# Performance work log

Hardware: AMD Instinct MI355X
Metric: run time of the kernel (lower is better)

## Reference

```python
import jax, jax.numpy as jnp
import numpy as np

DIM, HEADS, DH, M, PINV_ITERS, RES_K = 512, 8, 64, 256, 6, 33

def layernorm(x, w, b, eps=1e-5):
    mu = jnp.mean(x, -1, keepdims=True)
    var = jnp.var(x, -1, keepdims=True)
    return (x - mu) * jax.lax.rsqrt(var + eps) * w + b

def pinv_iter(x, iters=PINV_ITERS):
    # Moore-Penrose iterative pseudo-inverse (lucidrains nystrom-attention)
    ax = jnp.abs(x)
    z = jnp.swapaxes(x, -1, -2) / (jnp.max(ax.sum(-1)) * jnp.max(ax.sum(-2)))
    I = jnp.eye(x.shape[-1], dtype=x.dtype)
    for _ in range(iters):
        xz = x @ z
        z = 0.25 * z @ (13 * I - xz @ (15 * I - xz @ (7 * I - xz)))
    return z

def _core(x, w_qkv):
    b, n, _ = x.shape
    pad = (M - n % M) % M            # Nystrom pads at the FRONT to a multiple of m=256
    xp = jnp.pad(x, ((0, 0), (pad, 0), (0, 0)))
    npad = n + pad
    q, k, v = jnp.split(xp @ w_qkv, 3, axis=-1)
    split_heads = lambda t: t.reshape(b, npad, HEADS, DH).transpose(0, 2, 1, 3)
    q = split_heads(q) * (DH ** -0.5)
    k, v = split_heads(k), split_heads(v)
    l = npad // M                    # tokens per landmark
    q_l = q.reshape(b, HEADS, M, l, DH).mean(3)
    k_l = k.reshape(b, HEADS, M, l, DH).mean(3)
    return q, k, v, q_l, k_l, pad, n

def nystrom_out(x, w_qkv, w_out, b_out, res_kernel):
    q, k, v, q_l, k_l, pad, n = _core(x, w_qkv)
    attn1 = jax.nn.softmax(jnp.einsum('bhid,bhjd->bhij', q, k_l), -1)    # (b,h,N,M)
    attn2 = jax.nn.softmax(jnp.einsum('bhid,bhjd->bhij', q_l, k_l), -1)  # (b,h,M,M)
    attn3 = jax.nn.softmax(jnp.einsum('bhid,bhjd->bhij', q_l, k), -1)    # (b,h,M,N)
    out = (attn1 @ pinv_iter(attn2)) @ (attn3 @ v)
    # depthwise residual conv over sequence dim, per head
    out = out + jax.lax.conv_general_dilated(
        v, res_kernel, (1, 1), [(RES_K // 2, RES_K // 2), (0, 0)],
        dimension_numbers=('NCHW', 'OIHW', 'NCHW'), feature_group_count=HEADS)
    b = out.shape[0]
    out = out.transpose(0, 2, 1, 3).reshape(b, -1, HEADS * DH) @ w_out + b_out
    return out[:, -n:]

def nystrom_cls_row(x, w_qkv):
    # cls-token (query index pad, head 0) row of attn1 @ pinv(attn2) @ attn3;
    # identical math to the full (n x n) matrix row the torch code slices out.
    q, k, v, q_l, k_l, pad, n = _core(x, w_qkv)
    q0, k0, ql0, kl0 = q[:, 0], k[:, 0], q_l[:, 0], k_l[:, 0]
    attn2 = jax.nn.softmax(ql0 @ jnp.swapaxes(kl0, -1, -2), -1)   # (b,M,M)
    attn3 = jax.nn.softmax(ql0 @ jnp.swapaxes(k0, -1, -2), -1)    # (b,M,N)
    row1 = jax.nn.softmax(jnp.einsum('bd,bjd->bj', q0[:, pad], kl0), -1)
    row = jnp.einsum('bj,bjk->bk', row1, pinv_iter(attn2))
    row = jnp.einsum('bk,bkn->bn', row, attn3)                    # (b, N_padded)
    return row, pad

def dwconv(x, k, b, p):
    y = jax.lax.conv_general_dilated(x, k, (1, 1), [(p, p), (p, p)],
        dimension_numbers=('NCHW', 'OIHW', 'NCHW'), feature_group_count=x.shape[1])
    return y + b[None, :, None, None]

def leff(x, k7, b7, k5, b5, k3, b3, Hs, Ws):
    cls_t, feat = x[:, :1], x[:, 1:]
    B, N, C = feat.shape
    img = feat.transpose(0, 2, 1).reshape(B, C, Hs, Ws)
    y = dwconv(img, k7, b7, 3) + img + dwconv(img, k5, b5, 2) + dwconv(img, k3, b3, 1)
    y = y.reshape(B, C, Hs * Ws).transpose(0, 2, 1)
    return jnp.concatenate([cls_t, y], axis=1)

def setup_inputs():
    key = jax.random.key(0)
    ks = iter(jax.random.split(key, 32))
    n, n_classes = 22500, 2
    p = {}
    p['h'] = jax.random.normal(next(ks), (n, 1024), jnp.float32)
    p['fc1_w'] = jax.random.normal(next(ks), (1024, DIM), jnp.float32) * 0.02
    p['fc1_b'] = jnp.zeros((DIM,), jnp.float32)
    p['cls_token'] = jax.random.normal(next(ks), (1, 1, DIM), jnp.float32)
    for pre in ('l1', 'l2'):
        p[pre + '_ln_w'] = jnp.ones((DIM,), jnp.float32)
        p[pre + '_ln_b'] = jnp.zeros((DIM,), jnp.float32)
        p[pre + '_wqkv'] = jax.random.normal(next(ks), (DIM, 3 * HEADS * DH), jnp.float32) * 0.02
        p[pre + '_wout'] = jax.random.normal(next(ks), (HEADS * DH, DIM), jnp.float32) * 0.02
        p[pre + '_bout'] = jnp.zeros((DIM,), jnp.float32)
        p[pre + '_resk'] = jax.random.normal(next(ks), (HEADS, 1, RES_K, 1), jnp.float32) * 0.05
    for kk in (7, 5, 3):
        p['leff_k%d' % kk] = jax.random.normal(next(ks), (DIM, 1, kk, kk), jnp.float32) * 0.05
        p['leff_b%d' % kk] = jnp.zeros((DIM,), jnp.float32)
    p['norm_w'] = jnp.ones((DIM,), jnp.float32)
    p['norm_b'] = jnp.zeros((DIM,), jnp.float32)
    p['fc2_w'] = jax.random.normal(next(ks), (DIM, n_classes), jnp.float32) * 0.02
    p['fc2_b'] = jnp.zeros((n_classes,), jnp.float32)
    return p

def reference(h, fc1_w, fc1_b, cls_token,
              l1_ln_w, l1_ln_b, l1_wqkv, l1_wout, l1_bout, l1_resk,
              leff_k7, leff_b7, leff_k5, leff_b5, leff_k3, leff_b3,
              l2_ln_w, l2_ln_b, l2_wqkv, l2_wout, l2_bout, l2_resk,
              norm_w, norm_b, fc2_w, fc2_b):
    x = h[None]                                   # (1, n, 1024)
    n = x.shape[1]
    x = jax.nn.relu(x @ fc1_w + fc1_b)            # (1, n, 512)
    Hs = int(np.ceil(np.sqrt(n)))                 # 150 for n=22500
    add_len = Hs * Hs - n
    if add_len > 0:
        x = jnp.concatenate([x, x[:, :add_len]], axis=1)
    x = jnp.concatenate([jnp.broadcast_to(cls_token, (1, 1, DIM)), x], axis=1)
    # TransLayer 1
    x = x + nystrom_out(layernorm(x, l1_ln_w, l1_ln_b), l1_wqkv, l1_wout, l1_bout, l1_resk)
    # LeFF positional layer
    x = leff(x, leff_k7, leff_b7, leff_k5, leff_b5, leff_k3, leff_b3, Hs, Hs)
    # TransLayer 2 (first call in TransMIL.forward)
    h2 = x + nystrom_out(layernorm(x, l2_ln_w, l2_ln_b), l2_wqkv, l2_wout, l2_bout, l2_resk)
    # TransLayer 2 second call: residual update then attention matrix of updated state
    h3 = h2 + nystrom_out(layernorm(h2, l2_ln_w, l2_ln_b), l2_wqkv, l2_wout, l2_bout, l2_resk)
    row, pad = nystrom_cls_row(layernorm(h3, l2_ln_w, l2_ln_b), l2_wqkv)
    A = row[0, pad + 1: pad + 1 + n][:, None]     # (n, 1) cls->instance attention
    hf = layernorm(h2, norm_w, norm_b)[:, 0]      # (1, 512)
    logits = hf @ fc2_w + fc2_b                   # (1, n_classes)
    Y_prob = jax.nn.softmax(logits, -1)
    return logits, Y_prob, A
```

## Files before the change

### kernel.cpp

```cpp
#include <hip/hip_runtime.h>

#define NTOK 22500
#define N1   22501
#define NPAD 22528
#define PADR 27
#define DIM  512
#define NH   8
#define DHD  64
#define MM   256
#define LLM  88
#define HSZ  150
#define CSZ  256
#define NCH  88

typedef short bf16x8 __attribute__((ext_vector_type(8)));
typedef float f32x4  __attribute__((ext_vector_type(4)));
typedef unsigned short us;

union U8 { bf16x8 v; unsigned short u[8]; };

__device__ __forceinline__ unsigned short f2b(float f){
  unsigned int u = __float_as_uint(f);
  unsigned int r = u + 0x7fffu + ((u>>16)&1u);
  return (unsigned short)(r>>16);
}
__device__ __forceinline__ float bf2f(unsigned short u){
  return __uint_as_float(((unsigned int)u)<<16);
}
__device__ __forceinline__ bf16x8 cvt8(float4 a, float4 b){
  U8 u;
  u.u[0]=f2b(a.x); u.u[1]=f2b(a.y); u.u[2]=f2b(a.z); u.u[3]=f2b(a.w);
  u.u[4]=f2b(b.x); u.u[5]=f2b(b.y); u.u[6]=f2b(b.z); u.u[7]=f2b(b.w);
  return u.v;
}
__device__ __forceinline__ void gld16(const void* g, void* l){
  __builtin_amdgcn_global_load_lds(
      (const __attribute__((address_space(1))) void*)g,
      (__attribute__((address_space(3))) void*)l, 16, 0, 0);
}

__device__ __forceinline__ float waveSum(float v){
#pragma unroll
  for (int o=32;o>0;o>>=1) v += __shfl_down(v,o);
  return v;
}
__device__ __forceinline__ float waveMax(float v){
#pragma unroll
  for (int o=32;o>0;o>>=1) v = fmaxf(v,__shfl_down(v,o));
  return v;
}
__device__ __forceinline__ float blockSum256(float v, float* sb){
  v = waveSum(v);
  __syncthreads();
  if ((threadIdx.x&63)==0) sb[threadIdx.x>>6]=v;
  __syncthreads();
  return sb[0]+sb[1]+sb[2]+sb[3];
}
__device__ __forceinline__ float blockMax256(float v, float* sb){
  v = waveMax(v);
  __syncthreads();
  if ((threadIdx.x&63)==0) sb[threadIdx.x>>6]=v;
  __syncthreads();
  return fmaxf(fmaxf(sb[0],sb[1]),fmaxf(sb[2],sb[3]));
}

__global__ void k_wT(const float* __restrict__ W, us* __restrict__ Bt, int K, int N)
{
  __shared__ float tile[32][33];
  int tx = threadIdx.x&31, ty = threadIdx.x>>5;
  int k0 = blockIdx.x*32, n0 = blockIdx.y*32;
#pragma unroll
  for (int i=0;i<4;++i){
    int k = k0+ty+i*8;
    if (k<K && n0+tx<N) tile[ty+i*8][tx] = W[(size_t)k*N + n0+tx];
  }
  __syncthreads();
#pragma unroll
  for (int i=0;i<4;++i){
    int n = n0+ty+i*8, k = k0+tx;
    if (n<N && k<K) Bt[(size_t)n*K + k] = f2b(tile[tx][ty+i*8]);
  }
}

__global__ void k_vT(const us* __restrict__ V, us* __restrict__ Vt)
{
  __shared__ us tile[32][33];
  int tx = threadIdx.x&31, ty = threadIdx.x>>5;
  int p0 = blockIdx.x*32;
  int h = blockIdx.y>>1, d0 = (blockIdx.y&1)*32;
#pragma unroll
  for (int i=0;i<4;++i){
    int p = p0+ty+i*8;
    tile[ty+i*8][tx] = V[((size_t)h*NPAD+p)*DHD + d0+tx];
  }
  __syncthreads();
#pragma unroll
  for (int i=0;i<4;++i){
    int d = d0+ty+i*8;
    Vt[((size_t)h*DHD+d)*NPAD + p0+tx] = tile[tx][ty+i*8];
  }
}

template<int MODE>
__global__ __launch_bounds__(256) void k_gemm(const float* __restrict__ Af,
    const us* __restrict__ Ab, const us* __restrict__ Bt, const float* __restrict__ bias,
    us* __restrict__ Xb, float* __restrict__ Cf, float* __restrict__ C2,
    us* __restrict__ Q_, us* __restrict__ K_, us* __restrict__ V_,
    const us* __restrict__ zpg, int Kd)
{
  __shared__ us SM[16384];
  us* As = SM;
  us* Bs = SM + 8192;
  const int tid = threadIdx.x;
  const int m0 = blockIdx.x*128, n0 = blockIdx.y*128;
  const int lane = tid & 63;
  const int wid = tid >> 6;
  const int wm = (wid>>1)*64, wn = (wid&1)*64;
  f32x4 acc[4][4] = {};
  for (int k0=0; k0<Kd; k0+=64){
    __syncthreads();
    if (MODE==0){
#pragma unroll
      for (int i=0;i<8;++i){
        int g = i*256 + tid;
        int row = g>>4, k4 = (g&15)*4;
        int gm = m0 + row;
        ushort4 h4 = make_ushort4(0,0,0,0);
        if (gm < NTOK){
          float4 v = *(const float4*)(Af + (size_t)gm*Kd + k0 + k4);
          h4.x=f2b(v.x); h4.y=f2b(v.y); h4.z=f2b(v.z); h4.w=f2b(v.w);
        }
        *(ushort4*)(&As[row*64 + (k4 ^ ((row&7)<<3))]) = h4;
      }
    } else {
#pragma unroll
      for (int i=0;i<4;++i){
        int c = wid*4+i;
        int row = c*8 + (lane>>3);
        int scol8 = ((lane&7) ^ (row&7))*8;
        int gm = m0+row;
        const us* ga;
        if (MODE==2) ga = Ab + ((size_t)((gm<N1?gm:0)+PADR))*Kd + k0 + scol8;
        else ga = (gm>=PADR) ? Ab + (size_t)(gm-PADR)*Kd + k0 + scol8 : zpg + scol8;
        gld16(ga, &As[c*512]);
      }
    }
#pragma unroll
    for (int i=0;i<4;++i){
      int c = wid*4+i;
      int row = c*8 + (lane>>3);
      int scol8 = ((lane&7) ^ (row&7))*8;
      int vn = n0+row;
      if (MODE==3) vn = (vn<64)? vn : vn+448;
      gld16(Bt + (size_t)vn*Kd + k0 + scol8, &Bs[c*512]);
    }
    __syncthreads();
#pragma unroll
    for (int ks=0; ks<2; ++ks){
      const int kk = ks*32 + (lane>>4)*8;
      bf16x8 af[4], bfm[4];
#pragma unroll
      for (int t=0;t<4;++t){
        int r = wm + t*16 + (lane&15);
        af[t] = *(bf16x8*)(&As[r*64 + (kk ^ ((r&7)<<3))]);
        int c = wn + t*16 + (lane&15);
        bfm[t] = *(bf16x8*)(&Bs[c*64 + (kk ^ ((c&7)<<3))]);
      }
#pragma unroll
      for (int mt=0;mt<4;++mt)
#pragma unroll
        for (int nt=0;nt<4;++nt)
          acc[mt][nt] = __builtin_amdgcn_mfma_f32_16x16x32_bf16(af[mt], bfm[nt], acc[mt][nt], 0,0,0);
    }
  }
  const int rbase = (lane>>4)*4;
  const int cl = lane&15;
  if (MODE==3){
#pragma unroll
    for (int mt=0;mt<4;++mt)
#pragma unroll
      for (int r=0;r<4;++r){
        int gm = m0 + wm + mt*16 + rbase + r;
#pragma unroll
        for (int nt=0;nt<4;++nt){
          int gn = n0 + wn + nt*16 + cl;
          float v = acc[mt][nt][r];
          if (gn < 64) Cf[(size_t)gm*DHD + gn] = v*0.125f;
          else         C2[(size_t)gm*DHD + (gn-64)] = v;
        }
      }
    return;
  }
  const float sc1 = (MODE==1 && (blockIdx.y>>2)==0) ? 0.125f : 1.f;
  __syncthreads();
#pragma unroll
  for (int mt=0;mt<4;++mt)
#pragma unroll
    for (int r=0;r<4;++r){
      int row = wm + mt*16 + rbase + r;
#pragma unroll
      for (int nt=0;nt<4;++nt){
        int col = wn + nt*16 + cl;
        float v = acc[mt][nt][r];
        if (MODE==0){ v += bias[n0+col]; v = v>0.f?v:0.f; }
        else if (MODE==2){ v += bias[n0+col]; }
        else v *= sc1;
        SM[row*128 + col] = f2b(v);
      }
    }
  __syncthreads();
  if (MODE==1){
    const int sec = blockIdx.y>>2;
    us* dst = sec==0 ? Q_ : (sec==1 ? K_ : V_);
#pragma unroll
    for (int i=0;i<8;++i){
      int v8 = i*256 + tid;
      int row = v8>>4, c8 = (v8&15)*8;
      int gm = m0 + row, gn = n0 + c8;
      int hh = (gn>>6)&7, d = gn&63;
      *(bf16x8*)(dst + ((size_t)hh*NPAD+gm)*DHD + d) = *(bf16x8*)(&SM[row*128 + c8]);
    }
  } else if (MODE==0){
#pragma unroll
    for (int i=0;i<8;++i){
      int v8 = i*256 + tid;
      int row = v8>>4, c8 = (v8&15)*8;
      int gm = m0 + row;
      if (gm < NTOK)
        *(bf16x8*)(Xb + (size_t)(1+gm)*DIM + n0 + c8) = *(bf16x8*)(&SM[row*128 + c8]);
    }
  } else {
#pragma unroll
    for (int i=0;i<8;++i){
      int v8 = i*256 + tid;
      int row = v8>>4, c8 = (v8&15)*8;
      int gm = m0 + row;
      if (gm < N1){
        us* p = Xb + (size_t)gm*DIM + n0 + c8;
        U8 xo, ad, o;
        xo.v = *(bf16x8*)p;
        ad.v = *(bf16x8*)(&SM[row*128 + c8]);
#pragma unroll
        for (int j=0;j<8;++j) o.u[j] = f2b(bf2f(xo.u[j]) + bf2f(ad.u[j]));
        *(bf16x8*)p = o.v;
      }
    }
  }
}

__global__ void k_setcls(us* __restrict__ X, const float* __restrict__ cls){
  int i = blockIdx.x*256 + threadIdx.x;
  if (i < DIM) X[i] = f2b(cls[i]);
}
__global__ void k_copyu(us* __restrict__ d, const us* __restrict__ s, size_t n){
  size_t i = (size_t)blockIdx.x*256 + threadIdx.x;
  if (i<n) d[i]=s[i];
}

__global__ void k_ln(const us* __restrict__ X, us* __restrict__ Y,
                     const float* __restrict__ w, const float* __restrict__ b)
{
  __shared__ float sb[4];
  const us* x = X + (size_t)blockIdx.x*DIM;
  us* y = Y + (size_t)blockIdx.x*DIM;
  int t = threadIdx.x;
  ushort2 xv = *(const ushort2*)(x + 2*t);
  float a0=bf2f(xv.x), a1=bf2f(xv.y);
  float s = blockSum256(a0+a1, sb);
  float q = blockSum256(a0*a0+a1*a1, sb);
  float mean = s*(1.f/512.f);
  float var = q*(1.f/512.f) - mean*mean;
  float rstd = rsqrtf(var+1e-5f);
  float2 wv = *(const float2*)(w + 2*t);
  float2 bv = *(const float2*)(b + 2*t);
  ushort2 o;
  o.x = f2b((a0-mean)*rstd*wv.x+bv.x);
  o.y = f2b((a1-mean)*rstd*wv.y+bv.y);
  *(ushort2*)(y + 2*t) = o;
}

__global__ void k_landmark2(const us* __restrict__ Q, const us* __restrict__ K,
                            us* __restrict__ QL, us* __restrict__ KL)
{
  int hm = blockIdx.x;
  bool isK = hm >= NH*MM;
  if (isK) hm -= NH*MM;
  int h = hm>>8, m = hm&255; int d = threadIdx.x;
  const us* base = (isK?K:Q) + ((size_t)h*NPAD + (size_t)m*LLM)*DHD + d;
  float s = 0.f;
  for (int j=0;j<LLM;++j) s += bf2f(base[(size_t)j*DHD]);
  (isK?KL:QL)[((size_t)h*MM + m)*DHD + d] = f2b(s * (1.f/(float)LLM));
}
__global__ void k_landmark2f(const float* __restrict__ Q, const float* __restrict__ K,
                             float* __restrict__ QL, float* __restrict__ KL)
{
  int hm = blockIdx.x;
  bool isK = hm >= MM;
  int m = isK ? hm-MM : hm; int d = threadIdx.x;
  const float* base = (isK?K:Q) + (size_t)m*LLM*DHD + d;
  float s = 0.f;
  for (int j=0;j<LLM;++j) s += base[(size_t)j*DHD];
  (isK?KL:QL)[(size_t)m*DHD + d] = s * (1.f/(float)LLM);
}

__global__ __launch_bounds__(64) void k_nt64(const float* __restrict__ A,
    const float* __restrict__ B, float* __restrict__ C,
    long sA, long sB, long sC, int Nr)
{
  int lane = threadIdx.x;
  int n0 = blockIdx.x*64, m0 = blockIdx.y*64;
  A += (size_t)blockIdx.z*sA; B += (size_t)blockIdx.z*sB; C += (size_t)blockIdx.z*sC;
  f32x4 acc[4][4] = {};
#pragma unroll
  for (int ks=0;ks<2;++ks){
    int kk = ks*32 + (lane>>4)*8;
    bf16x8 af[4], bfr[4];
#pragma unroll
    for (int mt=0;mt<4;++mt){
      const float* p = A + (size_t)(m0+mt*16+(lane&15))*64 + kk;
      af[mt] = cvt8(*(const float4*)p, *(const float4*)(p+4));
    }
#pragma unroll
    for (int nt=0;nt<4;++nt){
      const float* p = B + (size_t)(n0+nt*16+(lane&15))*64 + kk;
      bfr[nt] = cvt8(*(const float4*)p, *(const float4*)(p+4));
    }
#pragma unroll
    for (int mt=0;mt<4;++mt)
#pragma unroll
      for (int nt=0;nt<4;++nt)
        acc[mt][nt] = __builtin_amdgcn_mfma_f32_16x16x32_bf16(af[mt], bfr[nt], acc[mt][nt], 0,0,0);
  }
#pragma unroll
  for (int mt=0;mt<4;++mt)
#pragma unroll
    for (int r=0;r<4;++r){
      int row = m0+mt*16+(lane>>4)*4+r;
#pragma unroll
      for (int nt=0;nt<4;++nt){
        int col = n0+nt*16+(lane&15);
        C[(size_t)row*Nr + col] = acc[mt][nt][r];
      }
    }
}

__global__ __launch_bounds__(64) void k_nt64b(const us* __restrict__ A,
    const us* __restrict__ B, float* __restrict__ C,
    long sA, long sB, long sC, int Nr)
{
  int lane = threadIdx.x;
  int n0 = blockIdx.x*64, m0 = blockIdx.y*64;
  A += (size_t)blockIdx.z*sA; B += (size_t)blockIdx.z*sB; C += (size_t)blockIdx.z*sC;
  f32x4 acc[4][4] = {};
#pragma unroll
  for (int ks=0;ks<2;++ks){
    int kk = ks*32 + (lane>>4)*8;
    bf16x8 af[4], bfr[4];
#pragma unroll
    for (int mt=0;mt<4;++mt)
      af[mt] = *(const bf16x8*)(A + (size_t)(m0+mt*16+(lane&15))*64 + kk);
#pragma unroll
    for (int nt=0;nt<4;++nt)
      bfr[nt] = *(const bf16x8*)(B + (size_t)(n0+nt*16+(lane&15))*64 + kk);
#pragma unroll
    for (int mt=0;mt<4;++mt)
#pragma unroll
      for (int nt=0;nt<4;++nt)
        acc[mt][nt] = __builtin_amdgcn_mfma_f32_16x16x32_bf16(af[mt], bfr[nt], acc[mt][nt], 0,0,0);
  }
#pragma unroll
  for (int mt=0;mt<4;++mt)
#pragma unroll
    for (int r=0;r<4;++r){
      int row = m0+mt*16+(lane>>4)*4+r;
#pragma unroll
      for (int nt=0;nt<4;++nt){
        int col = n0+nt*16+(lane&15);
        C[(size_t)row*Nr + col] = acc[mt][nt][r];
      }
    }
}

template<int PM>
__global__ __launch_bounds__(256) void k_pgemm(const us* __restrict__ A,
    const us* __restrict__ Bt, us* __restrict__ C, us* __restrict__ Ct,
    float dc, float alpha, int writeC)
{
  __shared__ us As[64*256];
  __shared__ us Bs[64*256];
  const int tid = threadIdx.x, lane = tid&63, wid = tid>>6;
  const int n0 = blockIdx.x*64, m0 = blockIdx.y*64;
  const us* Ab = A + (size_t)blockIdx.z*65536;
  const us* Bb = Bt + (size_t)blockIdx.z*(PM==2?16384:65536);
  for (int i=tid; i<4096; i+=256){
    int r = i>>6, c4 = (i&63)*4;
    *(ushort4*)(&As[r*256 + (c4 ^ ((r&7)<<3))]) = *(const ushort4*)(Ab + (size_t)(m0+r)*256 + c4);
    *(ushort4*)(&Bs[r*256 + (c4 ^ ((r&7)<<3))]) = *(const ushort4*)(Bb + (size_t)(n0+r)*256 + c4);
  }
  __syncthreads();
  const int wm = (wid>>1)*32, wn = (wid&1)*32;
  f32x4 acc[2][2] = {};
#pragma unroll
  for (int ks=0;ks<8;++ks){
    int kk = ks*32 + (lane>>4)*8;
    bf16x8 af[2], bfr[2];
#pragma unroll
    for (int t=0;t<2;++t){
      int rr = wm + t*16 + (lane&15);
      af[t] = *(const bf16x8*)(&As[rr*256 + (kk ^ ((rr&7)<<3))]);
      int cc = wn + t*16 + (lane&15);
      bfr[t] = *(const bf16x8*)(&Bs[cc*256 + (kk ^ ((cc&7)<<3))]);
    }
#pragma unroll
    for (int mt=0;mt<2;++mt)
#pragma unroll
      for (int nt=0;nt<2;++nt)
        acc[mt][nt] = __builtin_amdgcn_mfma_f32_16x16x32_bf16(af[mt], bfr[nt], acc[mt][nt], 0,0,0);
  }
#pragma unroll
  for (int mt=0;mt<2;++mt)
#pragma unroll
    for (int r=0;r<4;++r){
      int row = m0 + wm + mt*16 + (lane>>4)*4 + r;
#pragma unroll
      for (int nt=0;nt<2;++nt){
        int col = n0 + wn + nt*16 + (lane&15);
        float v = acc[mt][nt][r];
        if (PM==1) v = alpha*(dc*bf2f(Ab[(size_t)row*256+col]) - v);
        if (PM==2){
          Ct[(size_t)blockIdx.z*16384 + (size_t)col*256 + row] = f2b(v);
        } else {
          us bv = f2b(v);
          if (PM==0 || writeC) C[(size_t)blockIdx.z*65536 + (size_t)row*256 + col] = bv;
          Ct[(size_t)blockIdx.z*65536 + (size_t)col*256 + row] = bv;
        }
      }
    }
}

__global__ void k_softmax256(float* __restrict__ S, us* __restrict__ Sb)
{
  __shared__ float sb[4];
  float* row = S + ((size_t)blockIdx.x<<8);
  float x = row[threadIdx.x];
  float m = blockMax256(x, sb);
  float e = __expf(x-m);
  float s = blockSum256(e, sb);
  float p = e/s;
  row[threadIdx.x] = p;
  Sb[((size_t)blockIdx.x<<8) + threadIdx.x] = f2b(p);
}
__global__ void k_csmax(const float* __restrict__ A2, float* __restrict__ sums)
{
  __shared__ float sb[4];
  int b = blockIdx.x, j = threadIdx.x;
  const float* Ab = A2 + ((size_t)b<<16);
  float s = 0.f;
  for (int i=0;i<256;++i) s += Ab[((size_t)i<<8)+j];
  float m = blockMax256(s, sb);
  if (j==0) sums[b] = m;
}
__global__ void k_scale2(const float* __restrict__ sums, float* __restrict__ scl, int nb)
{
  __shared__ float sb[4];
  float m=-1e30f;
  for (int i=threadIdx.x;i<nb;i+=256) m = fmaxf(m, sums[i]);
  m = blockMax256(m, sb);
  if (threadIdx.x==0) scl[0] = 1.f/m;
}
__global__ void k_z0(const float* __restrict__ A2, us* __restrict__ Z, us* __restrict__ Zt,
                     const float* __restrict__ scl)
{
  size_t idx = (size_t)blockIdx.x*256 + threadIdx.x;
  size_t b = idx>>16; int i=(int)((idx>>8)&255), j=(int)(idx&255);
  float v = A2[idx]*scl[0];
  us bv = f2b(v);
  Zt[idx] = bv;
  Z[(b<<16)+((size_t)j<<8)+i] = bv;
}

__global__ __launch_bounds__(256) void k_attn3(const us* __restrict__ QLb,
    const us* __restrict__ Kb, const us* __restrict__ Vt,
    float* __restrict__ Pmax, float* __restrict__ Psum, us* __restrict__ Pacc)
{
  __shared__ us Ks[64*64];
  __shared__ us Vs[64*64];
  __shared__ us Ps[4*64*64];
  int h = blockIdx.y, cx = blockIdx.x;
  int tid = threadIdx.x, wid = tid>>6, lane = tid&63;
  bf16x8 aq[4][2];
#pragma unroll
  for (int mt=0;mt<4;++mt){
    const us* qp = QLb + ((size_t)h*MM + wid*64 + mt*16 + (lane&15))*DHD;
#pragma unroll
    for (int ks=0;ks<2;++ks)
      aq[mt][ks] = *(const bf16x8*)(qp + ks*32 + (lane>>4)*8);
  }
  float m_[4][4], l_[4][4];
  f32x4 acc[4][4] = {};
#pragma unroll
  for (int mt=0;mt<4;++mt)
#pragma unroll
    for (int r=0;r<4;++r){ m_[mt][r] = -1e30f; l_[mt][r] = 0.f; }

  us* Pw = &Ps[wid*4096];
  for (int t=0;t<4;++t){
    int kb0 = cx*CSZ + t*64;
    __syncthreads();
    for (int i=tid;i<1024;i+=256){
      int rr = i>>4, c4 = (i&15)*4;
      ushort4 ku = *(const ushort4*)(Kb + ((size_t)h*NPAD + kb0 + rr)*DHD + c4);
      *(ushort4*)(&Ks[rr*64 + (c4 ^ ((rr&7)<<3))]) = ku;
      ushort4 vu = *(const ushort4*)(Vt + ((size_t)h*DHD + rr)*NPAD + kb0 + c4);
      *(ushort4*)(&Vs[rr*64 + (c4 ^ ((rr&7)<<3))]) = vu;
    }
    __syncthreads();
    f32x4 s[4][4] = {};
#pragma unroll
    for (int ks=0;ks<2;++ks){
      int kk = ks*32 + (lane>>4)*8;
      bf16x8 kbf[4];
#pragma unroll
      for (int nt=0;nt<4;++nt){
        int key = nt*16 + (lane&15);
        kbf[nt] = *(const bf16x8*)(&Ks[key*64 + (kk ^ ((key&7)<<3))]);
      }
#pragma unroll
      for (int mt=0;mt<4;++mt)
#pragma unroll
        for (int nt=0;nt<4;++nt)
          s[mt][nt] = __builtin_amdgcn_mfma_f32_16x16x32_bf16(aq[mt][ks], kbf[nt], s[mt][nt], 0,0,0);
    }
#pragma unroll
    for (int mt=0;mt<4;++mt){
#pragma unroll
      for (int r=0;r<4;++r){
        float mx = fmaxf(fmaxf(s[mt][0][r], s[mt][1][r]), fmaxf(s[mt][2][r], s[mt][3][r]));
#pragma unroll
        for (int off=8;off>=1;off>>=1) mx = fmaxf(mx, __shfl_xor(mx, off));
        float mn = fmaxf(m_[mt][r], mx);
        float f = __expf(m_[mt][r]-mn);
        float la = 0.f;
#pragma unroll
        for (int nt=0;nt<4;++nt){ float p=__expf(s[mt][nt][r]-mn); s[mt][nt][r]=p; la+=p; }
#pragma unroll
        for (int off=8;off>=1;off>>=1) la += __shfl_xor(la, off);
        l_[mt][r] = l_[mt][r]*f + la;
        m_[mt][r] = mn;
#pragma unroll
        for (int dt=0;dt<4;++dt) acc[mt][dt][r] *= f;
      }
    }
#pragma unroll
    for (int mt=0;mt<4;++mt)
#pragma unroll
      for (int r=0;r<4;++r){
        int row = mt*16 + (lane>>4)*4 + r;
        int sw = (row&7)<<3;
#pragma unroll
        for (int nt=0;nt<4;++nt){
          int col = nt*16 + (lane&15);
          Pw[row*64 + (col ^ sw)] = f2b(s[mt][nt][r]);
        }
      }
#pragma unroll
    for (int ks=0;ks<2;++ks){
      int kk = ks*32 + (lane>>4)*8;
      bf16x8 pa[4], vb[4];
#pragma unroll
      for (int mt=0;mt<4;++mt){
        int arow = mt*16 + (lane&15);
        pa[mt] = *(const bf16x8*)(&Pw[arow*64 + (kk ^ ((arow&7)<<3))]);
      }
#pragma unroll
      for (int dt=0;dt<4;++dt){
        int d = dt*16 + (lane&15);
        vb[dt] = *(const bf16x8*)(&Vs[d*64 + (kk ^ ((d&7)<<3))]);
      }
#pragma unroll
      for (int mt=0;mt<4;++mt)
#pragma unroll
        for (int dt=0;dt<4;++dt)
          acc[mt][dt] = __builtin_amdgcn_mfma_f32_16x16x32_bf16(pa[mt], vb[dt], acc[mt][dt], 0,0,0);
    }
  }
  size_t pbase = ((size_t)h*NCH + cx)*MM;
#pragma unroll
  for (int mt=0;mt<4;++mt)
// ... 153 lines not shown
  for (int yy=0; yy<4; ++yy){
    int s = s0 + ty + yy*8;
    if (s < NTOK) tile[ty+yy*8][tx] = X[(size_t)(1+s)*DIM + c0+tx];
  }
  __syncthreads();
  for (int yy=0; yy<4; ++yy){
    int c = c0 + ty + yy*8;
    int s = s0 + tx;
    if (s < NTOK) T[(size_t)c*NTOK + s] = tile[tx][ty+yy*8];
  }
}
__global__ void k_tbwd(const us* __restrict__ T, us* __restrict__ X)
{
  __shared__ us tile[32][33];
  int tx = threadIdx.x & 31, ty = threadIdx.x >> 5;
  int s0 = blockIdx.x*32, c0 = blockIdx.y*32;
  for (int yy=0; yy<4; ++yy){
    int c = c0 + ty + yy*8, s = s0 + tx;
    if (s < NTOK) tile[ty+yy*8][tx] = T[(size_t)c*NTOK + s];
  }
  __syncthreads();
  for (int yy=0; yy<4; ++yy){
    int s = s0 + ty + yy*8, c = c0 + tx;
    if (s < NTOK) X[(size_t)(1+s)*DIM + c] = tile[tx][ty+yy*8];
  }
}
__global__ __launch_bounds__(256) void k_leff(const us* __restrict__ T,
    const float* __restrict__ k7, const float* __restrict__ b7,
    const float* __restrict__ k5, const float* __restrict__ b5,
    const float* __restrict__ k3, const float* __restrict__ b3,
    us* __restrict__ T2)
{
  __shared__ float tile[21*21];
  int c = blockIdx.y;
  int ti = blockIdx.x/10, tj = blockIdx.x%10;
  int i0 = ti*15-3, j0 = tj*15-3;
  const us* img = T + (size_t)c*NTOK;
  for (int idx=threadIdx.x; idx<441; idx+=256){
    int ii = idx/21, jj = idx%21;
    int gi = i0+ii, gj = j0+jj;
    tile[idx] = (gi>=0 && gi<HSZ && gj>=0 && gj<HSZ) ? bf2f(img[gi*HSZ+gj]) : 0.f;
  }
  __syncthreads();
  if (threadIdx.x < 225){
    int li = threadIdx.x/15, lj = threadIdx.x%15;
    int gi = ti*15+li, gj = tj*15+lj;
    float acc = tile[(li+3)*21 + (lj+3)] + b7[c]+b5[c]+b3[c];
    const float* w7 = k7 + c*49;
#pragma unroll
    for (int a=0;a<7;++a)
#pragma unroll
      for (int bb=0;bb<7;++bb) acc += tile[(li+a)*21 + (lj+bb)]*w7[a*7+bb];
    const float* w5 = k5 + c*25;
#pragma unroll
    for (int a=0;a<5;++a)
#pragma unroll
      for (int bb=0;bb<5;++bb) acc += tile[(li+1+a)*21 + (lj+1+bb)]*w5[a*5+bb];
    const float* w3 = k3 + c*9;
#pragma unroll
    for (int a=0;a<3;++a)
#pragma unroll
      for (int bb=0;bb<3;++bb) acc += tile[(li+2+a)*21 + (lj+2+bb)]*w3[a*3+bb];
    T2[(size_t)c*NTOK + gi*HSZ+gj] = f2b(acc);
  }
}

__global__ void k_row1(const float* __restrict__ Q0, const float* __restrict__ KL0,
                       float* __restrict__ row1)
{
  __shared__ float sb[4];
  __shared__ float qv[64];
  int t = threadIdx.x;
  if (t<64) qv[t] = Q0[PADR*DHD + t];
  __syncthreads();
  float l = 0.f;
#pragma unroll
  for (int d=0;d<64;++d) l += qv[d]*KL0[(size_t)t*DHD+d];
  float m = blockMax256(l, sb);
  float e = __expf(l-m);
  float s = blockSum256(e, sb);
  row1[t] = e/s;
}
__global__ void k_rz(const float* __restrict__ row1, const us* __restrict__ Zt,
                     float* __restrict__ rz)
{
  __shared__ float r1[256];
  int t = threadIdx.x;
  r1[t] = row1[t];
  __syncthreads();
  float s = 0.f;
  for (int k2=0;k2<256;++k2) s += r1[k2]*bf2f(Zt[(size_t)t*MM + k2]);
  rz[t] = s;
}
__global__ void k_rowstat(const float* __restrict__ L0, float* __restrict__ mx, float* __restrict__ se)
{
  __shared__ float sb[4];
  const float* row = L0 + (size_t)blockIdx.x*NPAD;
  float m = -1e30f;
  for (int i=threadIdx.x;i<NPAD;i+=256) m = fmaxf(m, row[i]);
  m = blockMax256(m, sb);
  float s = 0.f;
  for (int i=threadIdx.x;i<NPAD;i+=256) s += __expf(row[i]-m);
  s = blockSum256(s, sb);
  if (threadIdx.x==0){ mx[blockIdx.x]=m; se[blockIdx.x]=s; }
}
__global__ void k_aout(const float* __restrict__ L0, const float* __restrict__ rz,
    const float* __restrict__ mx, const float* __restrict__ se, float* __restrict__ out)
{
  __shared__ float wk[256], mk[256];
  int t = threadIdx.x;
  wk[t] = rz[t]/se[t];
  mk[t] = mx[t];
  __syncthreads();
  int p = blockIdx.x*256 + t;
  if (p >= NTOK) return;
  size_t pp = (size_t)(PADR+1+p);
  float a = 0.f;
  for (int k2=0;k2<256;++k2) a += wk[k2]*__expf(L0[(size_t)k2*NPAD+pp]-mk[k2]);
  out[4+p] = a;
}
__global__ void k_final(const us* __restrict__ H2r, const float* __restrict__ nw,
    const float* __restrict__ nbb, const float* __restrict__ w2, const float* __restrict__ b2,
    float* __restrict__ out)
{
  __shared__ float sb[4];
  __shared__ float hf[512];
  int t = threadIdx.x;
  float x0 = bf2f(H2r[t]), x1 = bf2f(H2r[256+t]);
  float s = blockSum256(x0+x1, sb);
  float q = blockSum256(x0*x0+x1*x1, sb);
  float mean = s*(1.f/512.f);
  float var = q*(1.f/512.f) - mean*mean;
  float rstd = rsqrtf(var+1e-5f);
  hf[t]     = (x0-mean)*rstd*nw[t]+nbb[t];
  hf[256+t] = (x1-mean)*rstd*nw[256+t]+nbb[256+t];
  __syncthreads();
  float p0 = hf[t]*w2[t*2]   + hf[256+t]*w2[(256+t)*2];
  float p1 = hf[t]*w2[t*2+1] + hf[256+t]*w2[(256+t)*2+1];
  p0 = blockSum256(p0, sb);
  p1 = blockSum256(p1, sb);
  if (t==0){
    float l0 = p0+b2[0], l1 = p1+b2[1];
    float m = fmaxf(l0,l1);
    float e0 = __expf(l0-m), e1 = __expf(l1-m), si = 1.f/(e0+e1);
    out[0]=l0; out[1]=l1; out[2]=e0*si; out[3]=e1*si;
  }
}

struct Bufs {
  float *A2,*sums,*scl,*Pmax,*Psum;
  us *Xb,*Yb,*OHb,*Qb,*Kb,*Vb,*Vtb,*QLb,*KLb,*A2b;
  us *Z0b,*Z0tb,*Z1b,*Z1tb,*XZb,*XZtb,*T1tb,*T2tb;
  us *A3Vtb,*WmT,*Pacc,*zpg;
};

static void run_pinv(const us* A2b, Bufs& b, int NB, hipStream_t st,
                     us** outZ, us** outZt)
{
  dim3 g(4,4,NB);
  us *Zc=b.Z0b, *Zct=b.Z0tb, *Zn=b.Z1b, *Znt=b.Z1tb;
  for (int it=0; it<6; ++it){
    k_pgemm<0><<<g,256,0,st>>>(A2b, Zct, b.XZb, b.XZtb, 0.f, 1.f, 1);
    k_pgemm<1><<<g,256,0,st>>>(b.XZb, b.XZtb, nullptr, b.T1tb, 7.f, 1.f, 0);
    k_pgemm<1><<<g,256,0,st>>>(b.XZb, b.T1tb, nullptr, b.T2tb, 15.f, 1.f, 0);
    k_pgemm<1><<<g,256,0,st>>>(Zc, b.T2tb, Zn, Znt, 13.f, 0.25f, 1);
    us* t1=Zc; Zc=Zn; Zn=t1;
    us* t2=Zct; Zct=Znt; Znt=t2;
  }
  *outZ = Zc; *outZt = Zct;
}

static void nystrom_layer(Bufs& b, const float* lnw, const float* lnb,
    const us* wqkvT, const us* woutT,
    const float* bout, const float* resk, hipStream_t st)
{
  k_ln<<<N1,256,0,st>>>(b.Xb, b.Yb, lnw, lnb);
  k_gemm<1><<<dim3(NPAD/128,12),256,0,st>>>(nullptr, b.Yb, wqkvT, nullptr,
      nullptr, nullptr, nullptr, b.Qb, b.Kb, b.Vb, b.zpg, DIM);
  k_vT<<<dim3(NPAD/32,16),256,0,st>>>(b.Vb, b.Vtb);
  k_landmark2<<<2*NH*MM,64,0,st>>>(b.Qb, b.Kb, b.QLb, b.KLb);
  k_nt64b<<<dim3(4,4,NH),64,0,st>>>(b.QLb, b.KLb, b.A2,
      (long)MM*DHD,(long)MM*DHD,(long)MM*MM, MM);
  k_softmax256<<<NH*MM,256,0,st>>>(b.A2, b.A2b);
  k_csmax<<<NH,256,0,st>>>(b.A2, b.sums);
  k_scale2<<<1,256,0,st>>>(b.sums, b.scl, NH);
  k_z0<<<NH*MM*MM/256,256,0,st>>>(b.A2, b.Z0b, b.Z0tb, b.scl);
  us *Zc, *Zct;
  run_pinv(b.A2b, b, NH, st, &Zc, &Zct);
  k_attn3<<<dim3(NCH,NH),256,0,st>>>(b.QLb, b.Kb, b.Vtb, b.Pmax, b.Psum, b.Pacc);
  k_attn3_merge<<<NH*MM,64,0,st>>>(b.Pmax, b.Psum, b.Pacc, b.A3Vtb);
  k_pgemm<2><<<dim3(1,4,NH),256,0,st>>>(Zc, b.A3Vtb, nullptr, b.WmT, 0.f, 1.f, 0);
  k_attn1<<<dim3(NPAD/64,NH),256,0,st>>>(b.Qb, b.KLb, b.WmT, b.OHb);
  k_seqconv<<<NPAD/SCBLK,256,0,st>>>(b.Vb, resk, b.OHb);
  k_gemm<2><<<dim3(176,4),256,0,st>>>(nullptr, b.OHb, woutT, bout,
      b.Xb, nullptr, nullptr, nullptr, nullptr, nullptr, b.zpg, DIM);
}

extern "C" void kernel_launch(void* const* d_in, const int* in_sizes, int n_in,
                              void* d_out, int out_size, void* d_ws, size_t ws_size,
                              hipStream_t stream)
{
  (void)n_in; (void)out_size;
  bool sig_order = (in_sizes[10] == 25088);
  int iL2 = sig_order ? 16 : 10;
  int iLf = sig_order ? 10 : 16;

  const float* h       = (const float*)d_in[0];
  const float* fc1_w   = (const float*)d_in[1];
  const float* fc1_b   = (const float*)d_in[2];
  const float* cls_tok = (const float*)d_in[3];
  const float* l1_lnw  = (const float*)d_in[4];
  const float* l1_lnb  = (const float*)d_in[5];
  const float* l1_wqkv = (const float*)d_in[6];
  const float* l1_wout = (const float*)d_in[7];
  const float* l1_bout = (const float*)d_in[8];
  const float* l1_resk = (const float*)d_in[9];
  const float* l2_lnw  = (const float*)d_in[iL2+0];
  const float* l2_lnb  = (const float*)d_in[iL2+1];
  const float* l2_wqkv = (const float*)d_in[iL2+2];
  const float* l2_wout = (const float*)d_in[iL2+3];
  const float* l2_bout = (const float*)d_in[iL2+4];
  const float* l2_resk = (const float*)d_in[iL2+5];
  const float* k7 = (const float*)d_in[iLf+0];
  const float* b7 = (const float*)d_in[iLf+1];
  const float* k5 = (const float*)d_in[iLf+2];
  const float* b5 = (const float*)d_in[iLf+3];
  const float* k3 = (const float*)d_in[iLf+4];
  const float* b3 = (const float*)d_in[iLf+5];
  const float* nw = (const float*)d_in[22];
  const float* nbb= (const float*)d_in[23];
  const float* w2 = (const float*)d_in[24];
  const float* b2 = (const float*)d_in[25];
  float* out = (float*)d_out;

  char* base = (char*)d_ws;
  auto allocF = [&](size_t n)->float*{
    float* p=(float*)base; base += ((n*sizeof(float)+255)&~(size_t)255); return p; };
  auto allocU = [&](size_t n)->us*{
    us* p=(us*)base; base += ((n*sizeof(us)+255)&~(size_t)255); return p; };

  const size_t S = (size_t)NPAD*DIM;
  const size_t SQ = (size_t)MM*MM;
  Bufs b;
  b.Xb  = allocU(S);
  b.Yb  = allocU(S);
  b.OHb = allocU(S);
  b.Qb  = allocU(S);
  b.Kb  = allocU(S);
  b.Vb  = allocU(S);
  b.Vtb = allocU(S);
  b.QLb = allocU((size_t)NH*MM*DHD);
  b.KLb = allocU((size_t)NH*MM*DHD);
  b.A2  = allocF((size_t)NH*SQ);
  b.A2b = allocU((size_t)NH*SQ);
  b.Z0b = allocU((size_t)NH*SQ);  b.Z0tb = allocU((size_t)NH*SQ);
  b.Z1b = allocU((size_t)NH*SQ);  b.Z1tb = allocU((size_t)NH*SQ);
  b.XZb = allocU((size_t)NH*SQ);  b.XZtb = allocU((size_t)NH*SQ);
  b.T1tb= allocU((size_t)NH*SQ);
  b.T2tb= allocU((size_t)NH*SQ);
  b.A3Vtb = allocU((size_t)NH*MM*DHD);
  b.WmT   = allocU((size_t)NH*MM*DHD);
  b.sums  = allocF(2*(size_t)NH*MM);
  b.scl   = allocF(16);
  b.Pmax  = allocF((size_t)NH*NCH*MM);
  b.Psum  = allocF((size_t)NH*NCH*MM);
  b.Pacc  = allocU((size_t)NH*NCH*MM*DHD);
  b.zpg   = allocU(512);
  us* fc1T   = allocU((size_t)DIM*1024);
  us* wqkvT1 = allocU((size_t)1536*DIM);
  us* wqkvT2 = allocU((size_t)1536*DIM);
  us* woutT1 = allocU((size_t)DIM*DIM);
  us* woutT2 = allocU((size_t)DIM*DIM);
  float* Q0   = allocF((size_t)NPAD*DHD);
  float* K0   = allocF((size_t)NPAD*DHD);
  float* QL0f = allocF((size_t)MM*DHD);
  float* KL0f = allocF((size_t)MM*DHD);
  float* row1 = allocF(256);
  float* rzv  = allocF(256);
  float* mxv  = allocF(256);
  float* sev  = allocF(256);
  us* h2row = allocU(512);
  if ((size_t)(base - (char*)d_ws) > ws_size) return;

  hipMemsetAsync((void*)b.zpg, 0, 1024, stream);

  k_wT<<<dim3(32,16),256,0,stream>>>(fc1_w, fc1T, 1024, DIM);
  k_wT<<<dim3(16,48),256,0,stream>>>(l1_wqkv, wqkvT1, DIM, 1536);
  k_wT<<<dim3(16,48),256,0,stream>>>(l2_wqkv, wqkvT2, DIM, 1536);
  k_wT<<<dim3(16,16),256,0,stream>>>(l1_wout, woutT1, DIM, DIM);
  k_wT<<<dim3(16,16),256,0,stream>>>(l2_wout, woutT2, DIM, DIM);

  k_gemm<0><<<dim3(176,4),256,0,stream>>>(h, nullptr, fc1T, fc1_b,
      b.Xb, nullptr, nullptr, nullptr, nullptr, nullptr, b.zpg, 1024);
  k_setcls<<<2,256,0,stream>>>(b.Xb, cls_tok);

  nystrom_layer(b, l1_lnw, l1_lnb, wqkvT1, woutT1, l1_bout, l1_resk, stream);
  k_tfwd<<<dim3(704,16),256,0,stream>>>(b.Xb, b.OHb);
  k_leff<<<dim3(100,512),256,0,stream>>>(b.OHb, k7,b7,k5,b5,k3,b3, b.Qb);
  k_tbwd<<<dim3(704,16),256,0,stream>>>(b.Qb, b.Xb);

  nystrom_layer(b, l2_lnw, l2_lnb, wqkvT2, woutT2, l2_bout, l2_resk, stream);
  k_copyu<<<2,256,0,stream>>>(h2row, b.Xb, 512);

  nystrom_layer(b, l2_lnw, l2_lnb, wqkvT2, woutT2, l2_bout, l2_resk, stream);

  k_ln<<<N1,256,0,stream>>>(b.Xb, b.Yb, l2_lnw, l2_lnb);
  k_gemm<3><<<dim3(176,1),256,0,stream>>>(nullptr, b.Yb, wqkvT2, nullptr,
      nullptr, Q0, K0, nullptr, nullptr, nullptr, b.zpg, DIM);
  k_landmark2f<<<2*MM,64,0,stream>>>(Q0, K0, QL0f, KL0f);
  k_nt64<<<dim3(4,4,1),64,0,stream>>>(QL0f, KL0f, b.A2, 0,0,0, MM);
  k_softmax256<<<MM,256,0,stream>>>(b.A2, b.A2b);
  k_csmax<<<1,256,0,stream>>>(b.A2, b.sums);
  k_scale2<<<1,256,0,stream>>>(b.sums, b.scl, 1);
  k_z0<<<MM*MM/256,256,0,stream>>>(b.A2, b.Z0b, b.Z0tb, b.scl);
  us *Zc, *Zct;
  run_pinv(b.A2b, b, 1, stream, &Zc, &Zct);
  k_row1<<<1,256,0,stream>>>(Q0, KL0f, row1);
  k_rz<<<1,256,0,stream>>>(row1, Zct, rzv);
  float* L0 = (float*)b.Yb;
  k_nt64<<<dim3(NPAD/64,4,1),64,0,stream>>>(QL0f, K0, L0, 0,0,0, NPAD);
  k_rowstat<<<MM,256,0,stream>>>(L0, mxv, sev);
  k_aout<<<88,256,0,stream>>>(L0, rzv, mxv, sev, out);
  k_final<<<1,256,0,stream>>>(h2row, nw, nbb, w2, b2, out);
}
```

Before: 2.487 ms.

## Fuse pinv iterations into one persistent kernel with grid barrier; add BM=64 GEMM tiles

Replaces the 24 separate pseudo-inverse GEMM launches per layer with a single persistent kernel. All tiles run every step and sync through an atomic grid barrier, which removes launch overhead and gaps between the small GEMMs. The generic GEMM also takes a BM template parameter with a flattened 1D grid, using 64-row tiles for the fc1, out-projection and cls QK GEMMs so more blocks are in flight. The grid barrier assumes all 128 blocks are co-resident, which holds for this grid size. After an even number of iterations the result lands back in the Z0 buffers, so downstream kernels read Z0.

```diff
diff --git a/kernel.cpp b/kernel.cpp
--- a/kernel.cpp
+++ b/kernel.cpp
@@ -64,6 +64,25 @@
   return fmaxf(fmaxf(sb[0],sb[1]),fmaxf(sb[2],sb[3]));
 }
 
+__device__ __forceinline__ void gridbar(unsigned* bcnt, unsigned* bgen)
+{
+  __syncthreads();
+  if (threadIdx.x==0){
+    __threadfence();
+    unsigned g = __hip_atomic_load(bgen, __ATOMIC_RELAXED, __HIP_MEMORY_SCOPE_AGENT);
+    unsigned v = __hip_atomic_fetch_add(bcnt, 1u, __ATOMIC_ACQ_REL, __HIP_MEMORY_SCOPE_AGENT);
+    if (v == gridDim.x-1u){
+      __hip_atomic_store(bcnt, 0u, __ATOMIC_RELAXED, __HIP_MEMORY_SCOPE_AGENT);
+      __hip_atomic_store(bgen, g+1u, __ATOMIC_RELEASE, __HIP_MEMORY_SCOPE_AGENT);
+    } else {
+      while (__hip_atomic_load(bgen, __ATOMIC_ACQUIRE, __HIP_MEMORY_SCOPE_AGENT) == g)
+        __builtin_amdgcn_s_sleep(8);
+    }
+    __threadfence();
+  }
+  __syncthreads();
+}
+
 __global__ void k_wT(const float* __restrict__ W, us* __restrict__ Bt, int K, int N)
 {
   __shared__ float tile[32][33];
@@ -101,27 +120,31 @@
   }
 }
 
-template<int MODE>
+template<int MODE, int BM>
 __global__ __launch_bounds__(256) void k_gemm(const float* __restrict__ Af,
     const us* __restrict__ Ab, const us* __restrict__ Bt, const float* __restrict__ bias,
     us* __restrict__ Xb, float* __restrict__ Cf, float* __restrict__ C2,
     us* __restrict__ Q_, us* __restrict__ K_, us* __restrict__ V_,
-    const us* __restrict__ zpg, int Kd)
-{
-  __shared__ us SM[16384];
+    const us* __restrict__ zpg, int Kd, int ntn)
+{
+  __shared__ us SM[BM*64 + 128*64];
   us* As = SM;
-  us* Bs = SM + 8192;
+  us* Bs = SM + BM*64;
   const int tid = threadIdx.x;
-  const int m0 = blockIdx.x*128, n0 = blockIdx.y*128;
+  const int bid = blockIdx.x;
+  const int ntile = bid % ntn;
+  const int m0 = (bid / ntn)*BM, n0 = ntile*128;
   const int lane = tid & 63;
   const int wid = tid >> 6;
-  const int wm = (wid>>1)*64, wn = (wid&1)*64;
-  f32x4 acc[4][4] = {};
+  constexpr int MT = BM/32;
+  constexpr int ACH = BM/32;
+  const int wm = (wid>>1)*(BM/2), wn = (wid&1)*64;
+  f32x4 acc[MT][4] = {};
   for (int k0=0; k0<Kd; k0+=64){
     __syncthreads();
     if (MODE==0){
 #pragma unroll
-      for (int i=0;i<8;++i){
+      for (int i=0;i<BM/16;++i){
         int g = i*256 + tid;
         int row = g>>4, k4 = (g&15)*4;
         int gm = m0 + row;
@@ -134,8 +157,8 @@
       }
     } else {
 #pragma unroll
-      for (int i=0;i<4;++i){
-        int c = wid*4+i;
+      for (int i=0;i<ACH;++i){
+        int c = wid*ACH+i;
         int row = c*8 + (lane>>3);
         int scol8 = ((lane&7) ^ (row&7))*8;
         int gm = m0+row;
@@ -158,16 +181,19 @@
 #pragma unroll
     for (int ks=0; ks<2; ++ks){
       const int kk = ks*32 + (lane>>4)*8;
-      bf16x8 af[4], bfm[4];
-#pragma unroll
-      for (int t=0;t<4;++t){
+      bf16x8 af[MT], bfm[4];
+#pragma unroll
+      for (int t=0;t<MT;++t){
         int r = wm + t*16 + (lane&15);
         af[t] = *(bf16x8*)(&As[r*64 + (kk ^ ((r&7)<<3))]);
+      }
+#pragma unroll
+      for (int t=0;t<4;++t){
         int c = wn + t*16 + (lane&15);
         bfm[t] = *(bf16x8*)(&Bs[c*64 + (kk ^ ((c&7)<<3))]);
       }
 #pragma unroll
-      for (int mt=0;mt<4;++mt)
+      for (int mt=0;mt<MT;++mt)
 #pragma unroll
         for (int nt=0;nt<4;++nt)
           acc[mt][nt] = __builtin_amdgcn_mfma_f32_16x16x32_bf16(af[mt], bfm[nt], acc[mt][nt], 0,0,0);
@@ -177,7 +203,7 @@
   const int cl = lane&15;
   if (MODE==3){
 #pragma unroll
-    for (int mt=0;mt<4;++mt)
+    for (int mt=0;mt<MT;++mt)
 #pragma unroll
       for (int r=0;r<4;++r){
         int gm = m0 + wm + mt*16 + rbase + r;
@@ -191,10 +217,10 @@
       }
     return;
   }
-  const float sc1 = (MODE==1 && (blockIdx.y>>2)==0) ? 0.125f : 1.f;
-  __syncthreads();
-#pragma unroll
-  for (int mt=0;mt<4;++mt)
+  const float sc1 = (MODE==1 && (ntile>>2)==0) ? 0.125f : 1.f;
+  __syncthreads();
+#pragma unroll
+  for (int mt=0;mt<MT;++mt)
 #pragma unroll
     for (int r=0;r<4;++r){
       int row = wm + mt*16 + rbase + r;
@@ -210,10 +236,10 @@
     }
   __syncthreads();
   if (MODE==1){
-    const int sec = blockIdx.y>>2;
+    const int sec = ntile>>2;
     us* dst = sec==0 ? Q_ : (sec==1 ? K_ : V_);
 #pragma unroll
-    for (int i=0;i<8;++i){
+    for (int i=0;i<BM/16;++i){
       int v8 = i*256 + tid;
       int row = v8>>4, c8 = (v8&15)*8;
       int gm = m0 + row, gn = n0 + c8;
@@ -222,7 +248,7 @@
     }
   } else if (MODE==0){
 #pragma unroll
-    for (int i=0;i<8;++i){
+    for (int i=0;i<BM/16;++i){
       int v8 = i*256 + tid;
       int row = v8>>4, c8 = (v8&15)*8;
       int gm = m0 + row;
@@ -231,7 +257,7 @@
     }
   } else {
 #pragma unroll
-    for (int i=0;i<8;++i){
+    for (int i=0;i<BM/16;++i){
       int v8 = i*256 + tid;
       int row = v8>>4, c8 = (v8&15)*8;
       int gm = m0 + row;
@@ -381,17 +407,14 @@
     }
 }
 
-template<int PM>
-__global__ __launch_bounds__(256) void k_pgemm(const us* __restrict__ A,
-    const us* __restrict__ Bt, us* __restrict__ C, us* __restrict__ Ct,
-    float dc, float alpha, int writeC)
-{
-  __shared__ us As[64*256];
-  __shared__ us Bs[64*256];
+__device__ void pgemm_tile(int PM, const us* __restrict__ A, const us* __restrict__ Bt,
+    us* __restrict__ C, us* __restrict__ Ct, float dc, float alpha, int writeC,
+    int head, int tile, us* As, us* Bs)
+{
   const int tid = threadIdx.x, lane = tid&63, wid = tid>>6;
-  const int n0 = blockIdx.x*64, m0 = blockIdx.y*64;
-  const us* Ab = A + (size_t)blockIdx.z*65536;
-  const us* Bb = Bt + (size_t)blockIdx.z*(PM==2?16384:65536);
+  const int n0 = (tile&3)*64, m0 = (tile>>2)*64;
+  const us* Ab = A + (size_t)head*65536;
+  const us* Bb = Bt + (size_t)head*65536;
   for (int i=tid; i<4096; i+=256){
     int r = i>>6, c4 = (i&63)*4;
     *(ushort4*)(&As[r*256 + (c4 ^ ((r&7)<<3))]) = *(const ushort4*)(Ab + (size_t)(m0+r)*256 + c4);
@@ -427,13 +450,80 @@
         int col = n0 + wn + nt*16 + (lane&15);
         float v = acc[mt][nt][r];
         if (PM==1) v = alpha*(dc*bf2f(Ab[(size_t)row*256+col]) - v);
-        if (PM==2){
-          Ct[(size_t)blockIdx.z*16384 + (size_t)col*256 + row] = f2b(v);
-        } else {
-          us bv = f2b(v);
-          if (PM==0 || writeC) C[(size_t)blockIdx.z*65536 + (size_t)row*256 + col] = bv;
-          Ct[(size_t)blockIdx.z*65536 + (size_t)col*256 + row] = bv;
-        }
+        us bv = f2b(v);
+        if (writeC) C[(size_t)head*65536 + (size_t)row*256 + col] = bv;
+        Ct[(size_t)head*65536 + (size_t)col*256 + row] = bv;
+      }
+    }
+}
+
+__global__ __launch_bounds__(256) void k_pinv(const us* __restrict__ A2,
+    us* __restrict__ Z0, us* __restrict__ Z0t, us* __restrict__ Z1, us* __restrict__ Z1t,
+    us* __restrict__ XZ, us* __restrict__ XZt, us* __restrict__ T1t, us* __restrict__ T2t,
+    unsigned* bcnt, unsigned* bgen)
+{
+  __shared__ us As[16384];
+  __shared__ us Bs[16384];
+  int head = blockIdx.x >> 4, tile = blockIdx.x & 15;
+  us *Zc=Z0, *Zct=Z0t, *Zn=Z1, *Znt=Z1t;
+  for (int it=0; it<6; ++it){
+    pgemm_tile(0, A2, Zct, XZ, XZt, 0.f, 1.f, 1, head, tile, As, Bs);
+    gridbar(bcnt, bgen);
+    pgemm_tile(1, XZ, XZt, nullptr, T1t, 7.f, 1.f, 0, head, tile, As, Bs);
+    gridbar(bcnt, bgen);
+    pgemm_tile(1, XZ, T1t, nullptr, T2t, 15.f, 1.f, 0, head, tile, As, Bs);
+    gridbar(bcnt, bgen);
+    pgemm_tile(1, Zc, T2t, Zn, Znt, 13.f, 0.25f, 1, head, tile, As, Bs);
+    gridbar(bcnt, bgen);
+    us* t1=Zc; Zc=Zn; Zn=t1;
+    us* t2=Zct; Zct=Znt; Znt=t2;
+  }
+}
+
+__global__ __launch_bounds__(256) void k_pgemm2(const us* __restrict__ A,
+    const us* __restrict__ Bt, us* __restrict__ Ct)
+{
+  __shared__ us As[16384];
+  __shared__ us Bs[16384];
+  const int tid = threadIdx.x, lane = tid&63, wid = tid>>6;
+  const int n0 = 0, m0 = blockIdx.y*64;
+  const us* Ab = A + (size_t)blockIdx.z*65536;
+  const us* Bb = Bt + (size_t)blockIdx.z*16384;
+  for (int i=tid; i<4096; i+=256){
+    int r = i>>6, c4 = (i&63)*4;
+    *(ushort4*)(&As[r*256 + (c4 ^ ((r&7)<<3))]) = *(const ushort4*)(Ab + (size_t)(m0+r)*256 + c4);
+    if (r < 64)
+      *(ushort4*)(&Bs[r*256 + (c4 ^ ((r&7)<<3))]) = *(const ushort4*)(Bb + (size_t)(n0+r)*256 + c4);
+  }
+  __syncthreads();
+  const int wm = (wid>>1)*32, wn = (wid&1)*32;
+  f32x4 acc[2][2] = {};
+#pragma unroll
+  for (int ks=0;ks<8;++ks){
+    int kk = ks*32 + (lane>>4)*8;
+    bf16x8 af[2], bfr[2];
+#pragma unroll
+    for (int t=0;t<2;++t){
+      int rr = wm + t*16 + (lane&15);
+      af[t] = *(const bf16x8*)(&As[rr*256 + (kk ^ ((rr&7)<<3))]);
+      int cc = wn + t*16 + (lane&15);
+      bfr[t] = *(const bf16x8*)(&Bs[cc*256 + (kk ^ ((cc&7)<<3))]);
+    }
+#pragma unroll
+    for (int mt=0;mt<2;++mt)
+#pragma unroll
+      for (int nt=0;nt<2;++nt)
+        acc[mt][nt] = __builtin_amdgcn_mfma_f32_16x16x32_bf16(af[mt], bfr[nt], acc[mt][nt], 0,0,0);
+  }
+#pragma unroll
+  for (int mt=0;mt<2;++mt)
+#pragma unroll
+    for (int r=0;r<4;++r){
+      int row = m0 + wm + mt*16 + (lane>>4)*4 + r;
+#pragma unroll
+      for (int nt=0;nt<2;++nt){
+        int col = n0 + wn + nt*16 + (lane&15);
+        Ct[(size_t)blockIdx.z*16384 + (size_t)col*256 + row] = f2b(acc[mt][nt][r]);
       }
     }
 }
@@ -893,31 +983,16 @@
   us *Xb,*Yb,*OHb,*Qb,*Kb,*Vb,*Vtb,*QLb,*KLb,*A2b;
   us *Z0b,*Z0tb,*Z1b,*Z1tb,*XZb,*XZtb,*T1tb,*T2tb;
   us *A3Vtb,*WmT,*Pacc,*zpg;
+  unsigned *bar;
 };
-
-static void run_pinv(const us* A2b, Bufs& b, int NB, hipStream_t st,
-                     us** outZ, us** outZt)
-{
-  dim3 g(4,4,NB);
-  us *Zc=b.Z0b, *Zct=b.Z0tb, *Zn=b.Z1b, *Znt=b.Z1tb;
-  for (int it=0; it<6; ++it){
-    k_pgemm<0><<<g,256,0,st>>>(A2b, Zct, b.XZb, b.XZtb, 0.f, 1.f, 1);
-    k_pgemm<1><<<g,256,0,st>>>(b.XZb, b.XZtb, nullptr, b.T1tb, 7.f, 1.f, 0);
-    k_pgemm<1><<<g,256,0,st>>>(b.XZb, b.T1tb, nullptr, b.T2tb, 15.f, 1.f, 0);
-    k_pgemm<1><<<g,256,0,st>>>(Zc, b.T2tb, Zn, Znt, 13.f, 0.25f, 1);
-    us* t1=Zc; Zc=Zn; Zn=t1;
-    us* t2=Zct; Zct=Znt; Znt=t2;
-  }
-  *outZ = Zc; *outZt = Zct;
-}
 
 static void nystrom_layer(Bufs& b, const float* lnw, const float* lnb,
     const us* wqkvT, const us* woutT,
     const float* bout, const float* resk, hipStream_t st)
 {
   k_ln<<<N1,256,0,st>>>(b.Xb, b.Yb, lnw, lnb);
-  k_gemm<1><<<dim3(NPAD/128,12),256,0,st>>>(nullptr, b.Yb, wqkvT, nullptr,
-      nullptr, nullptr, nullptr, b.Qb, b.Kb, b.Vb, b.zpg, DIM);
+  k_gemm<1,128><<<176*12,256,0,st>>>(nullptr, b.Yb, wqkvT, nullptr,
+      nullptr, nullptr, nullptr, b.Qb, b.Kb, b.Vb, b.zpg, DIM, 12);
   k_vT<<<dim3(NPAD/32,16),256,0,st>>>(b.Vb, b.Vtb);
   k_landmark2<<<2*NH*MM,64,0,st>>>(b.Qb, b.Kb, b.QLb, b.KLb);
   k_nt64b<<<dim3(4,4,NH),64,0,st>>>(b.QLb, b.KLb, b.A2,
@@ -926,15 +1001,15 @@
   k_csmax<<<NH,256,0,st>>>(b.A2, b.sums);
   k_scale2<<<1,256,0,st>>>(b.sums, b.scl, NH);
   k_z0<<<NH*MM*MM/256,256,0,st>>>(b.A2, b.Z0b, b.Z0tb, b.scl);
-  us *Zc, *Zct;
-  run_pinv(b.A2b, b, NH, st, &Zc, &Zct);
+  k_pinv<<<16*NH,256,0,st>>>(b.A2b, b.Z0b, b.Z0tb, b.Z1b, b.Z1tb,
+      b.XZb, b.XZtb, b.T1tb, b.T2tb, b.bar, b.bar+8);
   k_attn3<<<dim3(NCH,NH),256,0,st>>>(b.QLb, b.Kb, b.Vtb, b.Pmax, b.Psum, b.Pacc);
   k_attn3_merge<<<NH*MM,64,0,st>>>(b.Pmax, b.Psum, b.Pacc, b.A3Vtb);
-  k_pgemm<2><<<dim3(1,4,NH),256,0,st>>>(Zc, b.A3Vtb, nullptr, b.WmT, 0.f, 1.f, 0);
+  k_pgemm2<<<dim3(1,4,NH),256,0,st>>>(b.Z0b, b.A3Vtb, b.WmT);
   k_attn1<<<dim3(NPAD/64,NH),256,0,st>>>(b.Qb, b.KLb, b.WmT, b.OHb);
   k_seqconv<<<NPAD/SCBLK,256,0,st>>>(b.Vb, resk, b.OHb);
-  k_gemm<2><<<dim3(176,4),256,0,st>>>(nullptr, b.OHb, woutT, bout,
-      b.Xb, nullptr, nullptr, nullptr, nullptr, nullptr, b.zpg, DIM);
+  k_gemm<2,64><<<352*4,256,0,st>>>(nullptr, b.OHb, woutT, bout,
+      b.Xb, nullptr, nullptr, nullptr, nullptr, nullptr, b.zpg, DIM, 4);
 }
 
 extern "C" void kernel_launch(void* const* d_in, const int* in_sizes, int n_in,
@@ -1007,6 +1082,7 @@
   b.Psum  = allocF((size_t)NH*NCH*MM);
   b.Pacc  = allocU((size_t)NH*NCH*MM*DHD);
   b.zpg   = allocU(512);
+  b.bar   = (unsigned*)allocF(64);
   us* fc1T   = allocU((size_t)DIM*1024);
   us* wqkvT1 = allocU((size_t)1536*DIM);
   us* wqkvT2 = allocU((size_t)1536*DIM);
@@ -1024,6 +1100,7 @@
   if ((size_t)(base - (char*)d_ws) > ws_size) return;
 
   hipMemsetAsync((void*)b.zpg, 0, 1024, stream);
+  hipMemsetAsync((void*)b.bar, 0, 256, stream);
 
   k_wT<<<dim3(32,16),256,0,stream>>>(fc1_w, fc1T, 1024, DIM);
   k_wT<<<dim3(16,48),256,0,stream>>>(l1_wqkv, wqkvT1, DIM, 1536);
@@ -1031,8 +1108,8 @@
   k_wT<<<dim3(16,16),256,0,stream>>>(l1_wout, woutT1, DIM, DIM);
   k_wT<<<dim3(16,16),256,0,stream>>>(l2_wout, woutT2, DIM, DIM);
 
-  k_gemm<0><<<dim3(176,4),256,0,stream>>>(h, nullptr, fc1T, fc1_b,
-      b.Xb, nullptr, nullptr, nullptr, nullptr, nullptr, b.zpg, 1024);
+  k_gemm<0,64><<<352*4,256,0,stream>>>(h, nullptr, fc1T, fc1_b,
+      b.Xb, nullptr, nullptr, nullptr, nullptr, nullptr, b.zpg, 1024, 4);
   k_setcls<<<2,256,0,stream>>>(b.Xb, cls_tok);
 
   nystrom_layer(b, l1_lnw, l1_lnb, wqkvT1, woutT1, l1_bout, l1_resk, stream);
@@ -1046,18 +1123,18 @@
   nystrom_layer(b, l2_lnw, l2_lnb, wqkvT2, woutT2, l2_bout, l2_resk, stream);
 
   k_ln<<<N1,256,0,stream>>>(b.Xb, b.Yb, l2_lnw, l2_lnb);
-  k_gemm<3><<<dim3(176,1),256,0,stream>>>(nullptr, b.Yb, wqkvT2, nullptr,
-      nullptr, Q0, K0, nullptr, nullptr, nullptr, b.zpg, DIM);
+  k_gemm<3,64><<<352,256,0,stream>>>(nullptr, b.Yb, wqkvT2, nullptr,
+      nullptr, Q0, K0, nullptr, nullptr, nullptr, b.zpg, DIM, 1);
   k_landmark2f<<<2*MM,64,0,stream>>>(Q0, K0, QL0f, KL0f);
   k_nt64<<<dim3(4,4,1),64,0,stream>>>(QL0f, KL0f, b.A2, 0,0,0, MM);
   k_softmax256<<<MM,256,0,stream>>>(b.A2, b.A2b);
   k_csmax<<<1,256,0,stream>>>(b.A2, b.sums);
   k_scale2<<<1,256,0,stream>>>(b.sums, b.scl, 1);
   k_z0<<<MM*MM/256,256,0,stream>>>(b.A2, b.Z0b, b.Z0tb, b.scl);
-  us *Zc, *Zct;
-  run_pinv(b.A2b, b, 1, stream, &Zc, &Zct);
+  k_pinv<<<16,256,0,stream>>>(b.A2b, b.Z0b, b.Z0tb, b.Z1b, b.Z1tb,
+      b.XZb, b.XZtb, b.T1tb, b.T2tb, b.bar, b.bar+8);
   k_row1<<<1,256,0,stream>>>(Q0, KL0f, row1);
-  k_rz<<<1,256,0,stream>>>(row1, Zct, rzv);
+  k_rz<<<1,256,0,stream>>>(row1, b.Z0tb, rzv);
   float* L0 = (float*)b.Yb;
   k_nt64<<<dim3(NPAD/64,4,1),64,0,stream>>>(QL0f, K0, L0, 0,0,0, NPAD);
   k_rowstat<<<MM,256,0,stream>>>(L0, mxv, sev);
```

New measurement: 3.462 ms. 1.39x slower.
